# Kernel optimization log

Measured on AMD Instinct MI355X. Metric: run time of the kernel, lower is better.

Reference implementation:

```python
import jax, jax.numpy as jnp
import numpy as np

# Dims (match init_kwargs / input_specs)
N, N_REP, K, D = 8, 2048, 16, 3
C_IN, C_LIFT = 64, 64
C_MID = C_IN + C_LIFT   # 128
C_OUT = 128             # groups=C_OUT -> depthwise since C_MID == C_OUT
EPS = 1e-5


def setup_inputs() -> dict:
    key = jax.random.key(0)
    ks = jax.random.split(key, 10)
    w = lambda i, shape, fan_in: (jax.random.uniform(ks[i], shape, dtype=jnp.float32) * 2.0 - 1.0) / np.float32(np.sqrt(fan_in))
    return dict(
        p=jax.random.normal(ks[0], (N, N_REP, D), dtype=jnp.float32),
        P=jax.random.normal(ks[1], (N, N_REP, K, D), dtype=jnp.float32),
        F=jax.random.normal(ks[2], (N, N_REP, K, C_IN), dtype=jnp.float32),
        # BatchNorm over the D spatial channels (training-mode stats)
        bn_gamma=jnp.ones((D,), dtype=jnp.float32),
        bn_beta=jnp.zeros((D,), dtype=jnp.float32),
        # mlp_lift: Dense(D->C_LIFT) + Dense(C_LIFT->C_LIFT), ELU each
        lift_w1=w(3, (D, C_LIFT), D), lift_b1=jnp.zeros((C_LIFT,), dtype=jnp.float32),
        lift_w2=w(4, (C_LIFT, C_LIFT), C_LIFT), lift_b2=jnp.zeros((C_LIFT,), dtype=jnp.float32),
        # mid_conv: 1x1 Conv2d(D -> K) channels-last == Linear on last dim
        mid_w=w(5, (D, K), D), mid_b=jnp.zeros((K,), dtype=jnp.float32),
        # mlp: Dense(K->K) with ELU
        mlp_w=w(6, (K, K), K), mlp_b=jnp.zeros((K,), dtype=jnp.float32),
        # end_conv: Conv2d(C_MID -> C_OUT, kernel (K,1), groups=C_OUT) == depthwise
        # reduction over the neighbor dim; weight per (out_channel, neighbor)
        end_w=w(7, (C_OUT, K), K), end_b=jnp.zeros((C_OUT,), dtype=jnp.float32),
    )


def reference(p, P, F, bn_gamma, bn_beta, lift_w1, lift_b1, lift_w2, lift_b2,
              mid_w, mid_b, mlp_w, mlp_b, end_w, end_b):
    # Center neighborhoods on the representative point
    P_local = P - p[:, :, None, :]                              # (N,R,K,D)
    # Channels-last BatchNorm over D, batch stats over (N,R,K)
    mean = jnp.mean(P_local, axis=(0, 1, 2), keepdims=True)
    var = jnp.var(P_local, axis=(0, 1, 2), keepdims=True)
    P_norm = (P_local - mean) * jax.lax.rsqrt(var + EPS) * bn_gamma + bn_beta
    # Lift spatial coords to C_LIFT features (MLP of Dense+ELU layers)
    F_lift = jax.nn.elu(P_norm @ lift_w1 + lift_b1)
    F_lift = jax.nn.elu(F_lift @ lift_w2 + lift_b2)             # (N,R,K,C_LIFT)
    F_cat = jnp.concatenate([F_lift, F], axis=-1)               # (N,R,K,C_MID)
    # X-transform: 1x1 conv D->K then Dense(K->K)+ELU -> (N,R,K,K)
    X = P_norm @ mid_w + mid_b
    X = jax.nn.elu(X @ mlp_w + mlp_b)
    # Weighted aggregation: small batched matmul over the neighbor dim
    F_X = jnp.einsum('nrkj,nrjc->nrkc', X, F_cat)               # (N,R,K,C_MID)
    # Depthwise end conv: per-channel weighted sum over neighbors
    F_p = jnp.einsum('nrkc,ck->nrc', F_X, end_w) + end_b        # (N,R,C_OUT)
    return F_p
```

## Files before the change

### kernel.cpp

```cpp
#include <hip/hip_runtime.h>
#include <cstddef>

#define N_TOT   8
#define R_TOT   2048
#define KK      16
#define CL      64
#define CM      128
#define EPSV    1e-5f
#define CNTF    262144.0f

typedef float    f32x4  __attribute__((ext_vector_type(4)));
typedef short    bf16x8 __attribute__((ext_vector_type(8)));
typedef unsigned u32x4  __attribute__((ext_vector_type(4)));

union FragU { bf16x8 f; unsigned u[4]; };

__device__ float    g_w1f[72*4];
__device__ unsigned g_w2p[8*64*4];

__device__ __forceinline__ float elu_f(float x){
    return x > 0.f ? x : (__expf(x) - 1.f);
}

#if defined(__has_builtin) && __has_builtin(__builtin_amdgcn_cvt_pk_bf16_f32)
__device__ __forceinline__ unsigned pk_bf16(float a, float b){
    auto v = __builtin_amdgcn_cvt_pk_bf16_f32(a, b);
    unsigned u; __builtin_memcpy(&u, &v, 4);
    return u;
}
#else
__device__ __forceinline__ unsigned pk_bf16(float a, float b){
    unsigned ua = __float_as_uint(a), ub = __float_as_uint(b);
    ua += 0x7fff + ((ua >> 16) & 1);
    ub += 0x7fff + ((ub >> 16) & 1);
    return (ua >> 16) | (ub & 0xffff0000u);
}
#endif
__device__ __forceinline__ float bf_lo(unsigned u){ return __uint_as_float(u << 16); }
__device__ __forceinline__ float bf_hi(unsigned u){ return __uint_as_float(u & 0xffff0000u); }

__device__ __forceinline__ void split4(const float* x, unsigned* o){
    unsigned h01 = pk_bf16(x[0], x[1]);
    unsigned h23 = pk_bf16(x[2], x[3]);
    float l0 = x[0] - bf_lo(h01), l1 = x[1] - bf_hi(h01);
    float l2 = x[2] - bf_lo(h23), l3 = x[3] - bf_hi(h23);
    o[0] = h01; o[1] = h23; o[2] = pk_bf16(l0, l1); o[3] = pk_bf16(l2, l3);
}

__global__ __launch_bounds__(256) void xconv_stats(
    const float* __restrict__ p, const float* __restrict__ P,
    const float* __restrict__ w1, const float* __restrict__ b1,
    const float* __restrict__ w2, float* __restrict__ ws)
{
    const int tid = threadIdx.x;
    const int g = blockIdx.x*256 + tid;
    const float4* P4 = (const float4*)(P + (size_t)g*12);
    float4 a = P4[0], b = P4[1], c = P4[2];
    const int nr = g >> 2;
    float pp0 = p[nr*3], pp1 = p[nr*3+1], pp2 = p[nr*3+2];
    float vx0=a.x-pp0, vx1=a.w-pp0, vx2=b.z-pp0, vx3=c.y-pp0;
    float vy0=a.y-pp1, vy1=b.x-pp1, vy2=b.w-pp1, vy3=c.z-pp1;
    float vz0=a.z-pp2, vz1=b.y-pp2, vz2=c.x-pp2, vz3=c.w-pp2;
    float s1[3], s2[3];
    s1[0]=vx0+vx1+vx2+vx3; s2[0]=vx0*vx0+vx1*vx1+vx2*vx2+vx3*vx3;
    s1[1]=vy0+vy1+vy2+vy3; s2[1]=vy0*vy0+vy1*vy1+vy2*vy2+vy3*vy3;
    s1[2]=vz0+vz1+vz2+vz3; s2[2]=vz0*vz0+vz1*vz1+vz2*vz2+vz3*vz3;

    #pragma unroll
    for (int off = 32; off > 0; off >>= 1){
        #pragma unroll
        for (int d = 0; d < 3; d++){
            s1[d] += __shfl_down(s1[d], off, 64);
            s2[d] += __shfl_down(s2[d], off, 64);
        }
    }
    __shared__ float red[4][6];
    int wave = tid >> 6, lane = tid & 63;
    if (lane == 0){
        #pragma unroll
        for (int d = 0; d < 3; d++){ red[wave][d] = s1[d]; red[wave][3+d] = s2[d]; }
    }
    __syncthreads();
    float v = 0.f;
    if (tid < 6) v = red[0][tid] + red[1][tid] + red[2][tid] + red[3][tid];
    if (tid < 8) ws[blockIdx.x*8 + tid] = v;

    if (blockIdx.x == 0){
        if (wave == 0){
            f32x4 w4 = { w1[lane], w1[64+lane], w1[128+lane], b1[lane] };
            *(f32x4*)&g_w1f[((lane>>3)*9 + (lane&7))*4] = w4;
        } else if (wave == 1){
            const int lo16 = lane & 15, quad = lane >> 4;
            #pragma unroll
            for (int bb = 0; bb < 4; bb++)
                #pragma unroll
                for (int s = 0; s < 2; s++){
                    u32x4 f;
                    #pragma unroll
                    for (int d = 0; d < 4; d++){
                        int q0 = s*32 + quad*8 + d*2;
                        int idx = q0*64 + bb*16 + lo16;
                        f[d] = pk_bf16(w2[idx], w2[idx + 64]);
                    }
                    *(u32x4*)&g_w2p[((bb*2 + s)*64 + lane)*4] = f;
                }
        }
    }
}

__global__ __launch_bounds__(256) void xconv_main(
    const float* __restrict__ p,   const float* __restrict__ P,
    const float* __restrict__ F,
    const float* __restrict__ gamma,const float* __restrict__ beta,
    const float* __restrict__ mlpw,const float* __restrict__ mlpb,
    const float* __restrict__ midw,const float* __restrict__ midb,
    const float* __restrict__ b2,
    const float* __restrict__ endw,const float* __restrict__ endb,
    const float* __restrict__ ws,  float* __restrict__ out)
{
    __shared__ float    sEndw[128*20];
    __shared__ float    sW1f[72*4];
    __shared__ unsigned sW2[8*64*4];
    __shared__ float    sMid[16*4];

    const int tid  = threadIdx.x;
    const int lane = tid & 63;
    const int lo16 = lane & 15;
    const int quad = lane >> 4;
    const int wave = tid >> 6;

    if (wave == 0){
        *(f32x4*)&sW1f[lane*4] = *(const f32x4*)&g_w1f[lane*4];
        if (lane < 8)
            *(f32x4*)&sW1f[(64+lane)*4] = *(const f32x4*)&g_w1f[(64+lane)*4];
    } else if (wave == 1){
        #pragma unroll
        for (int i = 0; i < 8; i++)
            *(u32x4*)&sW2[(i*64+lane)*4] = *(const u32x4*)&g_w2p[(i*64+lane)*4];
    } else {
        int c = tid - 128;
        const f32x4* ep = (const f32x4*)endw;
        #pragma unroll
        for (int i = 0; i < 4; i++)
            *(f32x4*)&sEndw[c*20 + i*4] = ep[c*4 + i];
        if (c >= 112){
            int m2 = c - 112;
            f32x4 mv = { midw[m2], midw[16+m2], midw[32+m2], midb[m2] };
            *(f32x4*)&sMid[m2*4] = mv;
        }
    }

    float s1[3] = {0.f,0.f,0.f}, s2[3] = {0.f,0.f,0.f};
    {
        const f32x4* wp = (const f32x4*)ws;
        #pragma unroll
        for (int i = 0; i < 4; i++){
            int row = lane + i*64;
            f32x4 pa = wp[row*2], pb = wp[row*2 + 1];
            s1[0] += pa.x; s1[1] += pa.y; s1[2] += pa.z;
            s2[0] += pa.w; s2[1] += pb.x; s2[2] += pb.y;
        }
        #pragma unroll
        for (int off = 32; off > 0; off >>= 1){
            #pragma unroll
            for (int d = 0; d < 3; d++){
                s1[d] += __shfl_xor(s1[d], off, 64);
                s2[d] += __shfl_xor(s2[d], off, 64);
            }
        }
    }
    float sc[3], sh[3];
    #pragma unroll
    for (int d = 0; d < 3; d++){
        float mean = s1[d] * (1.0f/CNTF);
        float var  = s2[d] * (1.0f/CNTF) - mean*mean;
        float s    = gamma[d] * rsqrtf(var + EPSV);
        sc[d] = s; sh[d] = beta[d] - mean*s;
    }

    FragU mlpA[2];
    {
        float mw[4];
        #pragma unroll
        for (int r = 0; r < 4; r++) mw[r] = mlpw[(quad*4 + r)*16 + lo16];
        unsigned o[4]; split4(mw, o);
        mlpA[0].u[0]=o[0]; mlpA[0].u[1]=o[1]; mlpA[0].u[2]=o[0]; mlpA[0].u[3]=o[1];
        mlpA[1].u[0]=o[2]; mlpA[1].u[1]=o[3]; mlpA[1].u[2]=o[2]; mlpA[1].u[3]=o[3];
    }
    float mlpbr[4];
    #pragma unroll
    for (int r = 0; r < 4; r++) mlpbr[r] = mlpb[quad*4 + r];
    float b2r[4];
    #pragma unroll
    for (int b = 0; b < 4; b++) b2r[b] = b2[b*16 + lo16];
    const float endb0 = endb[lane], endb1 = endb[64 + lane];

    __syncthreads();

    const int wglobal = blockIdx.x*4 + wave;

    #pragma unroll 1
    for (int it = 0; it < 2; it++){
        const int nr = wglobal*2 + it;

        const int pb = nr*48 + lo16*3;
        float P0 = P[pb], P1 = P[pb+1], P2 = P[pb+2];
        float pp0 = p[nr*3], pp1 = p[nr*3+1], pp2 = p[nr*3+2];

        unsigned fh01[4], fh23[4];
        #pragma unroll
        for (int bt = 0; bt < 4; bt++){
            const size_t fb = (size_t)nr*1024 + (size_t)(quad*4)*64 + bt*16 + lo16;
            float f0 = F[fb], f1 = F[fb + 64], f2 = F[fb + 128], f3 = F[fb + 192];
            fh01[bt] = pk_bf16(f0, f1);
            fh23[bt] = pk_bf16(f2, f3);
        }

        const float pn0 = (P0 - pp0)*sc[0] + sh[0];
        const float pn1 = (P1 - pp1)*sc[1] + sh[1];
        const float pn2 = (P2 - pp2)*sc[2] + sh[2];

        FragU hf[2];
        #pragma unroll
        for (int s = 0; s < 2; s++){
            const f32x4* wp = (const f32x4*)&sW1f[((s*4 + quad)*9)*4];
            #pragma unroll
            for (int d = 0; d < 4; d++){
                f32x4 wa = wp[2*d], wb = wp[2*d+1];
                float h0  = fmaf(pn2, wa.z, fmaf(pn1, wa.y, fmaf(pn0, wa.x, wa.w)));
                float h1v = fmaf(pn2, wb.z, fmaf(pn1, wb.y, fmaf(pn0, wb.x, wb.w)));
                hf[s].u[d] = pk_bf16(elu_f(h0), elu_f(h1v));
            }
        }

        float x0[4];
        #pragma unroll
        for (int j = 0; j < 4; j++){
            f32x4 mw = *(const f32x4*)&sMid[(quad*4 + j)*4];
            x0[j] = fmaf(pn2, mw.z, fmaf(pn1, mw.y, fmaf(pn0, mw.x, mw.w)));
        }
        FragU x0f; split4(x0, x0f.u);

        f32x4 dx = {0.f,0.f,0.f,0.f};
        dx = __builtin_amdgcn_mfma_f32_16x16x32_bf16(mlpA[0].f, x0f.f, dx, 0,0,0);
        dx = __builtin_amdgcn_mfma_f32_16x16x32_bf16(mlpA[1].f, x0f.f, dx, 0,0,0);
        float xv[4];
        #pragma unroll
        for (int r = 0; r < 4; r++) xv[r] = elu_f(dx[r] + mlpbr[r]);
        FragU xA; split4(xv, xA.u);

        float o0 = 0.f, o1 = 0.f;

        #pragma unroll
        for (int b = 0; b < 4; b++){
            FragU wf0, wf1;
            *(u32x4*)wf0.u = *(const u32x4*)&sW2[((b*2 + 0)*64 + lane)*4];
            *(u32x4*)wf1.u = *(const u32x4*)&sW2[((b*2 + 1)*64 + lane)*4];
            f32x4 dl = {0.f,0.f,0.f,0.f};
            dl = __builtin_amdgcn_mfma_f32_16x16x32_bf16(hf[0].f, wf0.f, dl, 0,0,0);
            dl = __builtin_amdgcn_mfma_f32_16x16x32_bf16(hf[1].f, wf1.f, dl, 0,0,0);
            float fl[4];
            #pragma unroll
            for (int r = 0; r < 4; r++) fl[r] = elu_f(dl[r] + b2r[b]);
            FragU bfg;
            unsigned h01 = pk_bf16(fl[0], fl[1]), h23 = pk_bf16(fl[2], fl[3]);
            bfg.u[0] = h01; bfg.u[1] = h23; bfg.u[2] = h01; bfg.u[3] = h23;
            f32x4 da = {0.f,0.f,0.f,0.f};
            da = __builtin_amdgcn_mfma_f32_16x16x32_bf16(xA.f, bfg.f, da, 0,0,0);
            const float4 ew = *(const float4*)&sEndw[(b*16 + lo16)*20 + quad*4];
            float pt = da[0]*ew.x + da[1]*ew.y + da[2]*ew.z + da[3]*ew.w;
            pt += __shfl_xor(pt, 16, 64);
            pt += __shfl_xor(pt, 32, 64);
            if (b == quad) o0 = pt;
        }
        #pragma unroll
        for (int bt = 0; bt < 4; bt++){
            FragU bfg;
            bfg.u[0] = fh01[bt]; bfg.u[1] = fh23[bt];
            bfg.u[2] = fh01[bt]; bfg.u[3] = fh23[bt];
            f32x4 da = {0.f,0.f,0.f,0.f};
            da = __builtin_amdgcn_mfma_f32_16x16x32_bf16(xA.f, bfg.f, da, 0,0,0);
            const float4 ew = *(const float4*)&sEndw[(64 + bt*16 + lo16)*20 + quad*4];
            float pt = da[0]*ew.x + da[1]*ew.y + da[2]*ew.z + da[3]*ew.w;
            pt += __shfl_xor(pt, 16, 64);
            pt += __shfl_xor(pt, 32, 64);
            if (bt == quad) o1 = pt;
        }

        out[(size_t)nr*CM + lane]      = o0 + endb0;
        out[(size_t)nr*CM + 64 + lane] = o1 + endb1;
    }
}

extern "C" void kernel_launch(void* const* d_in, const int* in_sizes, int n_in,
                              void* d_out, int out_size, void* d_ws, size_t ws_size,
                              hipStream_t stream)
{
    const float* p     = (const float*)d_in[0];
    const float* P     = (const float*)d_in[1];
    const float* F     = (const float*)d_in[2];
    const float* gamma = (const float*)d_in[3];
    const float* beta  = (const float*)d_in[4];
    const float* w1    = (const float*)d_in[5];
    const float* b1    = (const float*)d_in[6];
    const float* w2    = (const float*)d_in[7];
    const float* b2    = (const float*)d_in[8];
    const float* midw  = (const float*)d_in[9];
    const float* midb  = (const float*)d_in[10];
    const float* mlpw  = (const float*)d_in[11];
    const float* mlpb  = (const float*)d_in[12];
    const float* endw  = (const float*)d_in[13];
    const float* endb  = (const float*)d_in[14];
    float* ws  = (float*)d_ws;
    float* out = (float*)d_out;

    xconv_stats<<<256, 256, 0, stream>>>(p, P, w1, b1, w2, ws);
    xconv_main <<<2048, 256, 0, stream>>>(p, P, F, gamma, beta, mlpw, mlpb,
                                          midw, midb, b2, endw, endb, ws, out);
}
```

Before: 148.7 us.

## Hoist BN stat reduction into tiny kernel and use one point per wave

Moves the final batch-norm statistics reduction out of every main-kernel block into a single 64-thread kernel that writes scale and shift to a device global. The main kernel then processes one representative point per wave instead of two, doubling the grid to 4096 blocks, and its launch bounds now request 5 blocks per CU. This removes redundant per-block reduction of the workspace and aims to raise occupancy and parallelism. In exchange it adds an extra kernel launch and doubles the per-block shared-weight staging overhead.

```diff
diff --git a/kernel.cpp b/kernel.cpp
--- a/kernel.cpp
+++ b/kernel.cpp
@@ -17,6 +17,7 @@
 
 __device__ float    g_w1f[72*4];
 __device__ unsigned g_w2p[8*64*4];
+__device__ float    g_bn[8];
 
 __device__ __forceinline__ float elu_f(float x){
     return x > 0.f ? x : (__expf(x) - 1.f);
@@ -108,15 +109,48 @@
     }
 }
 
-__global__ __launch_bounds__(256) void xconv_main(
+__global__ __launch_bounds__(64) void xconv_bn(
+    const float* __restrict__ ws,
+    const float* __restrict__ gamma, const float* __restrict__ beta)
+{
+    const int lane = threadIdx.x;
+    float s1[3] = {0.f,0.f,0.f}, s2[3] = {0.f,0.f,0.f};
+    const f32x4* wp = (const f32x4*)ws;
+    #pragma unroll
+    for (int i = 0; i < 4; i++){
+        int row = lane + i*64;
+        f32x4 pa = wp[row*2], pb = wp[row*2 + 1];
+        s1[0] += pa.x; s1[1] += pa.y; s1[2] += pa.z;
+        s2[0] += pa.w; s2[1] += pb.x; s2[2] += pb.y;
+    }
+    #pragma unroll
+    for (int off = 32; off > 0; off >>= 1){
+        #pragma unroll
+        for (int d = 0; d < 3; d++){
+            s1[d] += __shfl_xor(s1[d], off, 64);
+            s2[d] += __shfl_xor(s2[d], off, 64);
+        }
+    }
+    if (lane == 0){
+        #pragma unroll
+        for (int d = 0; d < 3; d++){
+            float mean = s1[d] * (1.0f/CNTF);
+            float var  = s2[d] * (1.0f/CNTF) - mean*mean;
+            float s    = gamma[d] * rsqrtf(var + EPSV);
+            g_bn[d] = s; g_bn[3+d] = beta[d] - mean*s;
+        }
+        g_bn[6] = 0.f; g_bn[7] = 0.f;
+    }
+}
+
+__global__ __launch_bounds__(256, 5) void xconv_main(
     const float* __restrict__ p,   const float* __restrict__ P,
     const float* __restrict__ F,
-    const float* __restrict__ gamma,const float* __restrict__ beta,
     const float* __restrict__ mlpw,const float* __restrict__ mlpb,
     const float* __restrict__ midw,const float* __restrict__ midb,
     const float* __restrict__ b2,
     const float* __restrict__ endw,const float* __restrict__ endb,
-    const float* __restrict__ ws,  float* __restrict__ out)
+    float* __restrict__ out)
 {
     __shared__ float    sEndw[128*20];
     __shared__ float    sW1f[72*4];
@@ -150,33 +184,9 @@
         }
     }
 
-    float s1[3] = {0.f,0.f,0.f}, s2[3] = {0.f,0.f,0.f};
-    {
-        const f32x4* wp = (const f32x4*)ws;
-        #pragma unroll
-        for (int i = 0; i < 4; i++){
-            int row = lane + i*64;
-            f32x4 pa = wp[row*2], pb = wp[row*2 + 1];
-            s1[0] += pa.x; s1[1] += pa.y; s1[2] += pa.z;
-            s2[0] += pa.w; s2[1] += pb.x; s2[2] += pb.y;
-        }
-        #pragma unroll
-        for (int off = 32; off > 0; off >>= 1){
-            #pragma unroll
-            for (int d = 0; d < 3; d++){
-                s1[d] += __shfl_xor(s1[d], off, 64);
-                s2[d] += __shfl_xor(s2[d], off, 64);
-            }
-        }
-    }
-    float sc[3], sh[3];
-    #pragma unroll
-    for (int d = 0; d < 3; d++){
-        float mean = s1[d] * (1.0f/CNTF);
-        float var  = s2[d] * (1.0f/CNTF) - mean*mean;
-        float s    = gamma[d] * rsqrtf(var + EPSV);
-        sc[d] = s; sh[d] = beta[d] - mean*s;
-    }
+    f32x4 bn0 = *(const f32x4*)&g_bn[0];
+    float sc0 = bn0.x, sc1 = bn0.y, sc2 = bn0.z, sh0 = bn0.w;
+    float sh1 = g_bn[4], sh2 = g_bn[5];
 
     FragU mlpA[2];
     {
@@ -197,99 +207,94 @@
 
     __syncthreads();
 
-    const int wglobal = blockIdx.x*4 + wave;
-
-    #pragma unroll 1
-    for (int it = 0; it < 2; it++){
-        const int nr = wglobal*2 + it;
-
-        const int pb = nr*48 + lo16*3;
-        float P0 = P[pb], P1 = P[pb+1], P2 = P[pb+2];
-        float pp0 = p[nr*3], pp1 = p[nr*3+1], pp2 = p[nr*3+2];
-
-        unsigned fh01[4], fh23[4];
-        #pragma unroll
-        for (int bt = 0; bt < 4; bt++){
-            const size_t fb = (size_t)nr*1024 + (size_t)(quad*4)*64 + bt*16 + lo16;
-            float f0 = F[fb], f1 = F[fb + 64], f2 = F[fb + 128], f3 = F[fb + 192];
-            fh01[bt] = pk_bf16(f0, f1);
-            fh23[bt] = pk_bf16(f2, f3);
-        }
-
-        const float pn0 = (P0 - pp0)*sc[0] + sh[0];
-        const float pn1 = (P1 - pp1)*sc[1] + sh[1];
-        const float pn2 = (P2 - pp2)*sc[2] + sh[2];
-
-        FragU hf[2];
-        #pragma unroll
-        for (int s = 0; s < 2; s++){
-            const f32x4* wp = (const f32x4*)&sW1f[((s*4 + quad)*9)*4];
-            #pragma unroll
-            for (int d = 0; d < 4; d++){
-                f32x4 wa = wp[2*d], wb = wp[2*d+1];
-                float h0  = fmaf(pn2, wa.z, fmaf(pn1, wa.y, fmaf(pn0, wa.x, wa.w)));
-                float h1v = fmaf(pn2, wb.z, fmaf(pn1, wb.y, fmaf(pn0, wb.x, wb.w)));
-                hf[s].u[d] = pk_bf16(elu_f(h0), elu_f(h1v));
-            }
-        }
-
-        float x0[4];
-        #pragma unroll
-        for (int j = 0; j < 4; j++){
-            f32x4 mw = *(const f32x4*)&sMid[(quad*4 + j)*4];
-            x0[j] = fmaf(pn2, mw.z, fmaf(pn1, mw.y, fmaf(pn0, mw.x, mw.w)));
-        }
-        FragU x0f; split4(x0, x0f.u);
-
-        f32x4 dx = {0.f,0.f,0.f,0.f};
-        dx = __builtin_amdgcn_mfma_f32_16x16x32_bf16(mlpA[0].f, x0f.f, dx, 0,0,0);
-        dx = __builtin_amdgcn_mfma_f32_16x16x32_bf16(mlpA[1].f, x0f.f, dx, 0,0,0);
-        float xv[4];
-        #pragma unroll
-        for (int r = 0; r < 4; r++) xv[r] = elu_f(dx[r] + mlpbr[r]);
-        FragU xA; split4(xv, xA.u);
-
-        float o0 = 0.f, o1 = 0.f;
-
-        #pragma unroll
-        for (int b = 0; b < 4; b++){
-            FragU wf0, wf1;
-            *(u32x4*)wf0.u = *(const u32x4*)&sW2[((b*2 + 0)*64 + lane)*4];
-            *(u32x4*)wf1.u = *(const u32x4*)&sW2[((b*2 + 1)*64 + lane)*4];
-            f32x4 dl = {0.f,0.f,0.f,0.f};
-            dl = __builtin_amdgcn_mfma_f32_16x16x32_bf16(hf[0].f, wf0.f, dl, 0,0,0);
-            dl = __builtin_amdgcn_mfma_f32_16x16x32_bf16(hf[1].f, wf1.f, dl, 0,0,0);
-            float fl[4];
-            #pragma unroll
-            for (int r = 0; r < 4; r++) fl[r] = elu_f(dl[r] + b2r[b]);
-            FragU bfg;
-            unsigned h01 = pk_bf16(fl[0], fl[1]), h23 = pk_bf16(fl[2], fl[3]);
-            bfg.u[0] = h01; bfg.u[1] = h23; bfg.u[2] = h01; bfg.u[3] = h23;
-            f32x4 da = {0.f,0.f,0.f,0.f};
-            da = __builtin_amdgcn_mfma_f32_16x16x32_bf16(xA.f, bfg.f, da, 0,0,0);
-            const float4 ew = *(const float4*)&sEndw[(b*16 + lo16)*20 + quad*4];
-            float pt = da[0]*ew.x + da[1]*ew.y + da[2]*ew.z + da[3]*ew.w;
-            pt += __shfl_xor(pt, 16, 64);
-            pt += __shfl_xor(pt, 32, 64);
-            if (b == quad) o0 = pt;
-        }
-        #pragma unroll
-        for (int bt = 0; bt < 4; bt++){
-            FragU bfg;
-            bfg.u[0] = fh01[bt]; bfg.u[1] = fh23[bt];
-            bfg.u[2] = fh01[bt]; bfg.u[3] = fh23[bt];
-            f32x4 da = {0.f,0.f,0.f,0.f};
-            da = __builtin_amdgcn_mfma_f32_16x16x32_bf16(xA.f, bfg.f, da, 0,0,0);
-            const float4 ew = *(const float4*)&sEndw[(64 + bt*16 + lo16)*20 + quad*4];
-            float pt = da[0]*ew.x + da[1]*ew.y + da[2]*ew.z + da[3]*ew.w;
-            pt += __shfl_xor(pt, 16, 64);
-            pt += __shfl_xor(pt, 32, 64);
-            if (bt == quad) o1 = pt;
-        }
-
-        out[(size_t)nr*CM + lane]      = o0 + endb0;
-        out[(size_t)nr*CM + 64 + lane] = o1 + endb1;
-    }
+    const int nr = blockIdx.x*4 + wave;
+
+    const int pb = nr*48 + lo16*3;
+    float P0 = P[pb], P1 = P[pb+1], P2 = P[pb+2];
+    float pp0 = p[nr*3], pp1 = p[nr*3+1], pp2 = p[nr*3+2];
+
+    unsigned fh01[4], fh23[4];
+    #pragma unroll
+    for (int bt = 0; bt < 4; bt++){
+        const size_t fb = (size_t)nr*1024 + (size_t)(quad*4)*64 + bt*16 + lo16;
+        float f0 = F[fb], f1 = F[fb + 64], f2 = F[fb + 128], f3 = F[fb + 192];
+        fh01[bt] = pk_bf16(f0, f1);
+        fh23[bt] = pk_bf16(f2, f3);
+    }
+
+    const float pn0 = (P0 - pp0)*sc0 + sh0;
+    const float pn1 = (P1 - pp1)*sc1 + sh1;
+    const float pn2 = (P2 - pp2)*sc2 + sh2;
+
+    FragU hf[2];
+    #pragma unroll
+    for (int s = 0; s < 2; s++){
+        const f32x4* wp = (const f32x4*)&sW1f[((s*4 + quad)*9)*4];
+        #pragma unroll
+        for (int d = 0; d < 4; d++){
+            f32x4 wa = wp[2*d], wb = wp[2*d+1];
+            float h0  = fmaf(pn2, wa.z, fmaf(pn1, wa.y, fmaf(pn0, wa.x, wa.w)));
+            float h1v = fmaf(pn2, wb.z, fmaf(pn1, wb.y, fmaf(pn0, wb.x, wb.w)));
+            hf[s].u[d] = pk_bf16(elu_f(h0), elu_f(h1v));
+        }
+    }
+
+    float x0[4];
+    #pragma unroll
+    for (int j = 0; j < 4; j++){
+        f32x4 mw = *(const f32x4*)&sMid[(quad*4 + j)*4];
+        x0[j] = fmaf(pn2, mw.z, fmaf(pn1, mw.y, fmaf(pn0, mw.x, mw.w)));
+    }
+    FragU x0f; split4(x0, x0f.u);
+
+    f32x4 dx = {0.f,0.f,0.f,0.f};
+    dx = __builtin_amdgcn_mfma_f32_16x16x32_bf16(mlpA[0].f, x0f.f, dx, 0,0,0);
+    dx = __builtin_amdgcn_mfma_f32_16x16x32_bf16(mlpA[1].f, x0f.f, dx, 0,0,0);
+    float xv[4];
+    #pragma unroll
+    for (int r = 0; r < 4; r++) xv[r] = elu_f(dx[r] + mlpbr[r]);
+    FragU xA; split4(xv, xA.u);
+
+    float o0 = 0.f, o1 = 0.f;
+
+    #pragma unroll
+    for (int b = 0; b < 4; b++){
+        FragU wf0, wf1;
+        *(u32x4*)wf0.u = *(const u32x4*)&sW2[((b*2 + 0)*64 + lane)*4];
+        *(u32x4*)wf1.u = *(const u32x4*)&sW2[((b*2 + 1)*64 + lane)*4];
+        f32x4 dl = {0.f,0.f,0.f,0.f};
+        dl = __builtin_amdgcn_mfma_f32_16x16x32_bf16(hf[0].f, wf0.f, dl, 0,0,0);
+        dl = __builtin_amdgcn_mfma_f32_16x16x32_bf16(hf[1].f, wf1.f, dl, 0,0,0);
+        float fl[4];
+        #pragma unroll
+        for (int r = 0; r < 4; r++) fl[r] = elu_f(dl[r] + b2r[b]);
+        FragU bfg;
+        unsigned h01 = pk_bf16(fl[0], fl[1]), h23 = pk_bf16(fl[2], fl[3]);
+        bfg.u[0] = h01; bfg.u[1] = h23; bfg.u[2] = h01; bfg.u[3] = h23;
+        f32x4 da = {0.f,0.f,0.f,0.f};
+        da = __builtin_amdgcn_mfma_f32_16x16x32_bf16(xA.f, bfg.f, da, 0,0,0);
+        const float4 ew = *(const float4*)&sEndw[(b*16 + lo16)*20 + quad*4];
+        float pt = da[0]*ew.x + da[1]*ew.y + da[2]*ew.z + da[3]*ew.w;
+        pt += __shfl_xor(pt, 16, 64);
+        pt += __shfl_xor(pt, 32, 64);
+        if (b == quad) o0 = pt;
+    }
+    #pragma unroll
+    for (int bt = 0; bt < 4; bt++){
+        FragU bfg;
+        bfg.u[0] = fh01[bt]; bfg.u[1] = fh23[bt];
+        bfg.u[2] = fh01[bt]; bfg.u[3] = fh23[bt];
+        f32x4 da = {0.f,0.f,0.f,0.f};
+        da = __builtin_amdgcn_mfma_f32_16x16x32_bf16(xA.f, bfg.f, da, 0,0,0);
+        const float4 ew = *(const float4*)&sEndw[(64 + bt*16 + lo16)*20 + quad*4];
+        float pt = da[0]*ew.x + da[1]*ew.y + da[2]*ew.z + da[3]*ew.w;
+        pt += __shfl_xor(pt, 16, 64);
+        pt += __shfl_xor(pt, 32, 64);
+        if (bt == quad) o1 = pt;
+    }
+
+    out[(size_t)nr*CM + lane]      = o0 + endb0;
+    out[(size_t)nr*CM + 64 + lane] = o1 + endb1;
 }
 
 extern "C" void kernel_launch(void* const* d_in, const int* in_sizes, int n_in,
@@ -315,6 +320,7 @@
     float* out = (float*)d_out;
 
     xconv_stats<<<256, 256, 0, stream>>>(p, P, w1, b1, w2, ws);
-    xconv_main <<<2048, 256, 0, stream>>>(p, P, F, gamma, beta, mlpw, mlpb,
-                                          midw, midb, b2, endw, endb, ws, out);
-}
+    xconv_bn   <<<1,    64, 0, stream>>>(ws, gamma, beta);
+    xconv_main <<<4096, 256, 0, stream>>>(p, P, F, mlpw, mlpb, midw, midb,
+                                          b2, endw, endb, out);
+}
```

Result: faster. 139.5 us (-6.2%).
